# Kernel optimization log

Measured on AMD Instinct MI355X. Metric: run time of the kernel, lower is better.

Reference implementation:

```python
import jax, jax.numpy as jnp
import numpy as np

B, T, C = 8, 2048, 1024
EXP = 4
EPS = 1e-6


def rmsnorm(x, w):
    xf = x.astype(jnp.float32)
    y = xf * jax.lax.rsqrt(jnp.mean(xf * xf, axis=-1, keepdims=True) + EPS)
    return y.astype(x.dtype) * w


def setup_inputs() -> dict:
    key = jax.random.key(0)
    ks = jax.random.split(key, 8)
    x = jax.random.normal(ks[0], (B, T, C), dtype=jnp.float32)
    norm1_w = jnp.ones((C,), jnp.float32)
    norm2_w = jnp.ones((C,), jnp.float32)
    s1 = 1.0 / np.sqrt(C)
    s2 = 1.0 / np.sqrt(EXP * C)
    mlp1_w = jax.random.uniform(ks[1], (C, C), jnp.float32, -s1, s1)  # stored (in,out)
    mlp1_b = jax.random.uniform(ks[2], (C,), jnp.float32, -s1, s1)
    mlp2_w1 = jax.random.uniform(ks[3], (C, EXP * C), jnp.float32, -s1, s1)
    mlp2_b1 = jax.random.uniform(ks[4], (EXP * C,), jnp.float32, -s1, s1)
    mlp2_w2 = jax.random.uniform(ks[5], (EXP * C, C), jnp.float32, -s2, s2)
    mlp2_b2 = jax.random.uniform(ks[6], (C,), jnp.float32, -s2, s2)
    return {"x": x, "norm1_w": norm1_w, "mlp1_w": mlp1_w, "mlp1_b": mlp1_b,
            "norm2_w": norm2_w, "mlp2_w1": mlp2_w1, "mlp2_b1": mlp2_b1,
            "mlp2_w2": mlp2_w2, "mlp2_b2": mlp2_b2}


def reference(x, norm1_w, mlp1_w, mlp1_b, norm2_w, mlp2_w1, mlp2_b1, mlp2_w2, mlp2_b2):
    Tdim = x.shape[-2]
    # linear-RNN cumulative state with triangular-number scaler (faithful to source)
    state = jnp.cumsum(rmsnorm(x, norm1_w), axis=1)
    scaler = jnp.cumsum(jnp.arange(1, Tdim + 1, dtype=x.dtype))[None, :, None]
    state = state / scaler
    gate = jax.nn.sigmoid(jnp.einsum('btc,cd->btd', state, mlp1_w) + mlp1_b)
    out = gate * x
    h = rmsnorm(out, norm2_w)
    h = jax.nn.relu(jnp.einsum('btc,ce->bte', h, mlp2_w1) + mlp2_b1)
    out = jnp.einsum('bte,ec->btc', h, mlp2_w2) + mlp2_b2 + out
    return out
```

## Files before the change

### kernel.cpp

```cpp
#include <hip/hip_runtime.h>

__device__ __forceinline__ float bf2f(unsigned short u) {
    union { unsigned int i; float f; } v;
    v.i = ((unsigned int)u) << 16;
    return v.f;
}
__device__ __forceinline__ unsigned short f2bf(float f) {
    union { float f; unsigned int i; } v;
    v.f = f;
    unsigned int r = (v.i + 0x7fffu + ((v.i >> 16) & 1u)) >> 16;
    return (unsigned short)r;
}

typedef __attribute__((ext_vector_type(8))) short short8;
typedef __attribute__((ext_vector_type(4))) float floatx4;

#define GLOBAL_AS __attribute__((address_space(1)))
#define LDS_AS __attribute__((address_space(3)))

static constexpr int Bdim = 8;
static constexpr int Tdim = 2048;
static constexpr int Cdim = 1024;
static constexpr int Edim = 4096;
static constexpr int Mdim = Bdim * Tdim;

__global__ __launch_bounds__(256) void transpose_f2b(
    const float* __restrict__ src, unsigned short* __restrict__ dst, int K, int N) {
    __shared__ float tile[32][33];
    int n0 = blockIdx.x * 32;
    int k0 = blockIdx.y * 32;
    int tx = threadIdx.x & 31;
    int ty = threadIdx.x >> 5;
#pragma unroll
    for (int i = 0; i < 32; i += 8)
        tile[ty + i][tx] = src[(size_t)(k0 + ty + i) * N + n0 + tx];
    __syncthreads();
#pragma unroll
    for (int i = 0; i < 32; i += 8)
        dst[(size_t)(n0 + ty + i) * K + k0 + tx] = f2bf(tile[tx][ty + i]);
}

__global__ __launch_bounds__(256) void rms_inv_kernel(
    const float* __restrict__ x, float* __restrict__ rinv) {
    int row = blockIdx.x;
    int tid = threadIdx.x;
    float4 v = ((const float4*)(x + (size_t)row * Cdim))[tid];
    float s = v.x * v.x + v.y * v.y + v.z * v.z + v.w * v.w;
#pragma unroll
    for (int o = 32; o > 0; o >>= 1) s += __shfl_down(s, o, 64);
    __shared__ float ps[4];
    if ((tid & 63) == 0) ps[tid >> 6] = s;
    __syncthreads();
    if (tid == 0) {
        float tot = ps[0] + ps[1] + ps[2] + ps[3];
        rinv[row] = rsqrtf(tot * (1.0f / (float)Cdim) + 1e-6f);
    }
}

__global__ __launch_bounds__(256) void chunk_sums(
    const float* __restrict__ x, const float* __restrict__ rinv,
    const float* __restrict__ w, float* __restrict__ P) {
    int idx = blockIdx.x;
    int cb = idx & 3;
    int k = (idx >> 2) & 31;
    int b = idx >> 7;
    int c = cb * 256 + threadIdx.x;
    float wc = w[c];
    const float* base = x + ((size_t)b * Tdim + k * 64) * Cdim + c;
    const float* rbase = rinv + (size_t)b * Tdim + k * 64;
    float s = 0.f;
#pragma unroll 8
    for (int t = 0; t < 64; t++) s += base[(size_t)t * Cdim] * rbase[t];
    P[((size_t)b * 32 + k) * Cdim + c] = s * wc;
}

__global__ __launch_bounds__(256) void chunk_scan(float* __restrict__ P) {
    int g = blockIdx.x * 256 + threadIdx.x;
    int b = g >> 10;
    int c = g & 1023;
    float* p = P + (size_t)b * 32 * Cdim + c;
    float run = 0.f;
#pragma unroll
    for (int k = 0; k < 32; k++) {
        float v = p[(size_t)k * Cdim];
        p[(size_t)k * Cdim] = run;
        run += v;
    }
}

__global__ __launch_bounds__(256) void cumsum_state(
    const float* __restrict__ x, const float* __restrict__ rinv,
    const float* __restrict__ w, const float* __restrict__ P,
    unsigned short* __restrict__ state) {
    int idx = blockIdx.x;
    int cb = idx & 3;
    int k = (idx >> 2) & 31;
    int b = idx >> 7;
    int c = cb * 256 + threadIdx.x;
    float wc = w[c];
    float acc = P[((size_t)b * 32 + k) * Cdim + c];
    const float* base = x + ((size_t)b * Tdim + k * 64) * Cdim + c;
    const float* rbase = rinv + (size_t)b * Tdim + k * 64;
    unsigned short* sbase = state + ((size_t)b * Tdim + k * 64) * Cdim + c;
#pragma unroll 4
    for (int t = 0; t < 64; t++) {
        acc += base[(size_t)t * Cdim] * rbase[t] * wc;
        int tt = k * 64 + t;
        float inv = 2.0f / ((float)(tt + 1) * (float)(tt + 2));
        sbase[(size_t)t * Cdim] = f2bf(acc * inv);
    }
}

__global__ __launch_bounds__(256) void rmsnorm_f2b(
    const float* __restrict__ x, const float* __restrict__ w,
    unsigned short* __restrict__ y) {
    int row = blockIdx.x;
    int tid = threadIdx.x;
    float4 v = ((const float4*)(x + (size_t)row * Cdim))[tid];
    float s = v.x * v.x + v.y * v.y + v.z * v.z + v.w * v.w;
#pragma unroll
    for (int o = 32; o > 0; o >>= 1) s += __shfl_down(s, o, 64);
    __shared__ float ps[4];
    if ((tid & 63) == 0) ps[tid >> 6] = s;
    __syncthreads();
    float tot = ps[0] + ps[1] + ps[2] + ps[3];
    float r = rsqrtf(tot * (1.0f / (float)Cdim) + 1e-6f);
    float4 w4 = ((const float4*)w)[tid];
    ushort4 o;
    o.x = f2bf(v.x * r * w4.x);
    o.y = f2bf(v.y * r * w4.y);
    o.z = f2bf(v.z * r * w4.z);
    o.w = f2bf(v.w * r * w4.w);
    ((ushort4*)(y + (size_t)row * Cdim))[tid] = o;
}

template <int EPI>
__global__ __launch_bounds__(256) void gemm_bt(
    const unsigned short* __restrict__ A, const unsigned short* __restrict__ BT,
    const float* __restrict__ bias, const float* __restrict__ extra,
    void* __restrict__ Coutv, int M, int N, int K) {
    __shared__ __attribute__((aligned(16))) unsigned short As[2][128 * 32];
    __shared__ __attribute__((aligned(16))) unsigned short Bs[2][128 * 32];

    int tid = threadIdx.x;
    int bn = blockIdx.x, bm = blockIdx.y;
    int wave = tid >> 6, lane = tid & 63;
    int wm = (wave & 1) * 64, wn = (wave >> 1) * 64;
    int lrow = lane & 15;
    int lk = (lane >> 4) << 3;

    const unsigned short* Abase = A + (size_t)bm * 128 * K;
    const unsigned short* Bbase = BT + (size_t)bn * 128 * K;

    floatx4 acc[4][4] = {};

    int qrow = tid >> 2;
    int qcol = (tid & 3) << 3;
    const unsigned short* ArowLo = Abase + (size_t)qrow * K + qcol;
    const unsigned short* ArowHi = Abase + (size_t)(qrow + 64) * K + qcol;
    const unsigned short* BrowLo = Bbase + (size_t)qrow * K + qcol;
    const unsigned short* BrowHi = Bbase + (size_t)(qrow + 64) * K + qcol;

#define STAGE(buf, koff)                                                                   \
    do {                                                                                   \
        __builtin_amdgcn_global_load_lds((const GLOBAL_AS void*)(ArowLo + (koff)),         \
                                         (LDS_AS void*)(As[buf] + (size_t)tid * 8), 16, 0, 0); \
        __builtin_amdgcn_global_load_lds((const GLOBAL_AS void*)(ArowHi + (koff)),         \
                                         (LDS_AS void*)(As[buf] + (size_t)(tid + 256) * 8), 16, 0, 0); \
        __builtin_amdgcn_global_load_lds((const GLOBAL_AS void*)(BrowLo + (koff)),         \
                                         (LDS_AS void*)(Bs[buf] + (size_t)tid * 8), 16, 0, 0); \
        __builtin_amdgcn_global_load_lds((const GLOBAL_AS void*)(BrowHi + (koff)),         \
                                         (LDS_AS void*)(Bs[buf] + (size_t)(tid + 256) * 8), 16, 0, 0); \
    } while (0)

    int iters = K >> 5;
    STAGE(0, 0);
    for (int k = 0; k < iters; k++) {
        int cur = k & 1;
        __syncthreads();
        if (k + 1 < iters) STAGE(cur ^ 1, (k + 1) << 5);

        short8 af[4], bfr[4];
#pragma unroll
        for (int i = 0; i < 4; i++)
            af[i] = *(const short8*)(As[cur] + (wm + i * 16 + lrow) * 32 + lk);
#pragma unroll
        for (int j = 0; j < 4; j++)
            bfr[j] = *(const short8*)(Bs[cur] + (wn + j * 16 + lrow) * 32 + lk);
#pragma unroll
        for (int i = 0; i < 4; i++)
#pragma unroll
            for (int j = 0; j < 4; j++)
                acc[i][j] = __builtin_amdgcn_mfma_f32_16x16x32_bf16(af[i], bfr[j], acc[i][j], 0, 0, 0);
    }
#undef STAGE

    int crow = (lane >> 4) * 4;
    int ccol = lane & 15;
#pragma unroll
    for (int i = 0; i < 4; i++) {
#pragma unroll
        for (int j = 0; j < 4; j++) {
            size_t gm = (size_t)bm * 128 + wm + i * 16 + crow;
            size_t gn = (size_t)bn * 128 + wn + j * 16 + ccol;
            float bsv = bias[gn];
#pragma unroll
            for (int r = 0; r < 4; r++) {
                float v = acc[i][j][r] + bsv;
                size_t off = (gm + r) * (size_t)N + gn;
                if (EPI == 0) {
                    float g = 1.f / (1.f + __expf(-v));
                    ((float*)Coutv)[off] = g * extra[off];
                } else if (EPI == 1) {
                    ((unsigned short*)Coutv)[off] = f2bf(v > 0.f ? v : 0.f);
                } else {
                    ((float*)Coutv)[off] = v + extra[off];
                }
            }
        }
    }
}

extern "C" void kernel_launch(void* const* d_in, const int* in_sizes, int n_in,
                              void* d_out, int out_size, void* d_ws, size_t ws_size,
                              hipStream_t stream) {
    const float* x   = (const float*)d_in[0];
    const float* n1w = (const float*)d_in[1];
    const float* w1  = (const float*)d_in[2];
    const float* b1  = (const float*)d_in[3];
    const float* n2w = (const float*)d_in[4];
    const float* w21 = (const float*)d_in[5];
    const float* b21 = (const float*)d_in[6];
    const float* w22 = (const float*)d_in[7];
    const float* b22 = (const float*)d_in[8];
    float* out = (float*)d_out;

    char* ws = (char*)d_ws;
    const size_t MB = 1024ull * 1024ull;
    unsigned short* state = (unsigned short*)(ws);
    unsigned short* w1T   = (unsigned short*)(ws + 32 * MB);
    unsigned short* w21T  = (unsigned short*)(ws + 34 * MB);
    unsigned short* w22T  = (unsigned short*)(ws + 42 * MB);
    float* P              = (float*)(ws + 50 * MB);
    float* rinv           = (float*)(ws + 51 * MB);
    unsigned short* h     = (unsigned short*)(ws + 52 * MB);
    float* out1 = out;

    int slice_rows = Mdim;
    while (52 * MB + (size_t)slice_rows * Edim * 2 > ws_size && slice_rows > 1024)
        slice_rows >>= 1;

    transpose_f2b<<<dim3(Cdim / 32, Cdim / 32), 256, 0, stream>>>(w1, w1T, Cdim, Cdim);
    transpose_f2b<<<dim3(Edim / 32, Cdim / 32), 256, 0, stream>>>(w21, w21T, Cdim, Edim);
    transpose_f2b<<<dim3(Cdim / 32, Edim / 32), 256, 0, stream>>>(w22, w22T, Edim, Cdim);

    rms_inv_kernel<<<Mdim, 256, 0, stream>>>(x, rinv);

    chunk_sums<<<1024, 256, 0, stream>>>(x, rinv, n1w, P);
    chunk_scan<<<32, 256, 0, stream>>>(P);
    cumsum_state<<<1024, 256, 0, stream>>>(x, rinv, n1w, P, state);

    gemm_bt<0><<<dim3(Cdim / 128, Mdim / 128), 256, 0, stream>>>(
        state, w1T, b1, x, out1, Mdim, Cdim, Cdim);

    rmsnorm_f2b<<<Mdim, 256, 0, stream>>>(out1, n2w, state);

    for (int m0 = 0; m0 < Mdim; m0 += slice_rows) {
        gemm_bt<1><<<dim3(Edim / 128, slice_rows / 128), 256, 0, stream>>>(
            state + (size_t)m0 * Cdim, w21T, b21, nullptr, h, slice_rows, Edim, Cdim);
        gemm_bt<2><<<dim3(Cdim / 128, slice_rows / 128), 256, 0, stream>>>(
            h, w22T, b22, out1 + (size_t)m0 * Cdim, out + (size_t)m0 * Cdim,
            slice_rows, Cdim, Edim);
    }
}
```

Baseline: 649.3 us.

## Rewrite GEMM with 256x128 tiles, triple-buffered LDS, swizzle and XCD remap

Replaces the 128x128 double-buffered bf16 GEMM with a 512-thread 256x128 tile kernel. It uses BK=64, a three-stage LDS ring filled by global_load_lds, and an XOR swizzle to avoid LDS bank conflicts. A 1D grid is remapped so consecutive blocks land on the same XCD for L2 reuse, and loads are interleaved with MFMA halves using barriers and setprio. The aim is higher MFMA utilization and better latency hiding, at the cost of much more LDS (144KB) per block and tricky waitcnt ordering.

```diff
diff --git a/kernel.cpp b/kernel.cpp
--- a/kernel.cpp
+++ b/kernel.cpp
@@ -135,74 +135,129 @@
 }
 
 template <int EPI>
-__global__ __launch_bounds__(256) void gemm_bt(
+__global__ __launch_bounds__(512, 2) void gemm8(
     const unsigned short* __restrict__ A, const unsigned short* __restrict__ BT,
     const float* __restrict__ bias, const float* __restrict__ extra,
-    void* __restrict__ Coutv, int M, int N, int K) {
-    __shared__ __attribute__((aligned(16))) unsigned short As[2][128 * 32];
-    __shared__ __attribute__((aligned(16))) unsigned short Bs[2][128 * 32];
+    void* __restrict__ Coutv, int N, int K) {
+    __shared__ __attribute__((aligned(16))) unsigned short As[3][256 * 64];
+    __shared__ __attribute__((aligned(16))) unsigned short Bs[3][128 * 64];
 
     int tid = threadIdx.x;
-    int bn = blockIdx.x, bm = blockIdx.y;
-    int wave = tid >> 6, lane = tid & 63;
-    int wm = (wave & 1) * 64, wn = (wave >> 1) * 64;
+    int nbn = N >> 7;
+    int id = blockIdx.x;
+    int nwg = gridDim.x;
+    if ((nwg & 7) == 0) id = (id & 7) * (nwg >> 3) + (id >> 3);
+    int bn = id % nbn;
+    int bm = id / nbn;
+
+    int lane = tid & 63;
+    int w = tid >> 6;
+    int wm = w & 3;
+    int wn = w >> 2;
     int lrow = lane & 15;
-    int lk = (lane >> 4) << 3;
-
-    const unsigned short* Abase = A + (size_t)bm * 128 * K;
+    int l4 = lane >> 4;
+    int swz = lrow & 7;
+
+    const unsigned short* Abase = A + (size_t)bm * 256 * K;
     const unsigned short* Bbase = BT + (size_t)bn * 128 * K;
 
+    int sr = tid >> 3;
+    int col8 = (tid & 7) ^ (sr & 7);
+
+#define STAGE_A(sb, u, k0)                                                               \
+    __builtin_amdgcn_global_load_lds(                                                    \
+        (const GLOBAL_AS void*)(Abase + (size_t)((u) * 64 + sr) * K + (k0) + col8 * 8),  \
+        (LDS_AS void*)(As[sb] + (u) * 4096 + tid * 8), 16, 0, 0)
+#define STAGE_B(sb, u, k0)                                                               \
+    __builtin_amdgcn_global_load_lds(                                                    \
+        (const GLOBAL_AS void*)(Bbase + (size_t)((u) * 64 + sr) * K + (k0) + col8 * 8),  \
+        (LDS_AS void*)(Bs[sb] + (u) * 4096 + tid * 8), 16, 0, 0)
+
     floatx4 acc[4][4] = {};
-
-    int qrow = tid >> 2;
-    int qcol = (tid & 3) << 3;
-    const unsigned short* ArowLo = Abase + (size_t)qrow * K + qcol;
-    const unsigned short* ArowHi = Abase + (size_t)(qrow + 64) * K + qcol;
-    const unsigned short* BrowLo = Bbase + (size_t)qrow * K + qcol;
-    const unsigned short* BrowHi = Bbase + (size_t)(qrow + 64) * K + qcol;
-
-#define STAGE(buf, koff)                                                                   \
-    do {                                                                                   \
-        __builtin_amdgcn_global_load_lds((const GLOBAL_AS void*)(ArowLo + (koff)),         \
-                                         (LDS_AS void*)(As[buf] + (size_t)tid * 8), 16, 0, 0); \
-        __builtin_amdgcn_global_load_lds((const GLOBAL_AS void*)(ArowHi + (koff)),         \
-                                         (LDS_AS void*)(As[buf] + (size_t)(tid + 256) * 8), 16, 0, 0); \
-        __builtin_amdgcn_global_load_lds((const GLOBAL_AS void*)(BrowLo + (koff)),         \
-                                         (LDS_AS void*)(Bs[buf] + (size_t)tid * 8), 16, 0, 0); \
-        __builtin_amdgcn_global_load_lds((const GLOBAL_AS void*)(BrowHi + (koff)),         \
-                                         (LDS_AS void*)(Bs[buf] + (size_t)(tid + 256) * 8), 16, 0, 0); \
-    } while (0)
-
-    int iters = K >> 5;
-    STAGE(0, 0);
-    for (int k = 0; k < iters; k++) {
-        int cur = k & 1;
-        __syncthreads();
-        if (k + 1 < iters) STAGE(cur ^ 1, (k + 1) << 5);
-
-        short8 af[4], bfr[4];
+    int nt = K >> 6;
+
+    STAGE_A(0, 0, 0); STAGE_A(0, 1, 0); STAGE_A(0, 2, 0); STAGE_A(0, 3, 0);
+    STAGE_B(0, 0, 0); STAGE_B(0, 1, 0);
+    STAGE_A(1, 0, 64); STAGE_A(1, 1, 64); STAGE_A(1, 2, 64); STAGE_A(1, 3, 64);
+    STAGE_B(1, 0, 64); STAGE_B(1, 1, 64);
+    asm volatile("s_waitcnt vmcnt(6)" ::: "memory");
+    __builtin_amdgcn_s_barrier();
+
+    int buf = 0;
+    for (int t = 0; t < nt; t++) {
+        const unsigned short* Ab = As[buf];
+        const unsigned short* Bb = Bs[buf];
+        int sb = buf + 2; if (sb >= 3) sb -= 3;
+        int k2 = (t + 2) << 6;
+        bool st = (t + 2) < nt;
+
+        short8 af[4][2], bfr[2][2];
 #pragma unroll
         for (int i = 0; i < 4; i++)
-            af[i] = *(const short8*)(As[cur] + (wm + i * 16 + lrow) * 32 + lk);
-#pragma unroll
-        for (int j = 0; j < 4; j++)
-            bfr[j] = *(const short8*)(Bs[cur] + (wn + j * 16 + lrow) * 32 + lk);
+#pragma unroll
+            for (int ks = 0; ks < 2; ks++)
+                af[i][ks] = *(const short8*)(Ab + (wm * 64 + i * 16 + lrow) * 64 +
+                                             (((ks * 4 + l4) ^ swz) << 3));
+#pragma unroll
+        for (int j = 0; j < 2; j++)
+#pragma unroll
+            for (int ks = 0; ks < 2; ks++)
+                bfr[j][ks] = *(const short8*)(Bb + (wn * 64 + j * 16 + lrow) * 64 +
+                                              (((ks * 4 + l4) ^ swz) << 3));
+        if (st) { STAGE_A(sb, 0, k2); STAGE_A(sb, 1, k2); STAGE_A(sb, 2, k2); }
+        asm volatile("s_waitcnt lgkmcnt(8)" ::: "memory");
+        __builtin_amdgcn_s_barrier();
+        asm volatile("s_waitcnt lgkmcnt(0)" ::: "memory");
+        __builtin_amdgcn_s_setprio(1);
 #pragma unroll
         for (int i = 0; i < 4; i++)
 #pragma unroll
-            for (int j = 0; j < 4; j++)
-                acc[i][j] = __builtin_amdgcn_mfma_f32_16x16x32_bf16(af[i], bfr[j], acc[i][j], 0, 0, 0);
-    }
-#undef STAGE
-
-    int crow = (lane >> 4) * 4;
+            for (int j = 0; j < 2; j++)
+#pragma unroll
+                for (int ks = 0; ks < 2; ks++)
+                    acc[i][j] = __builtin_amdgcn_mfma_f32_16x16x32_bf16(
+                        af[i][ks], bfr[j][ks], acc[i][j], 0, 0, 0);
+        __builtin_amdgcn_s_setprio(0);
+        __builtin_amdgcn_s_barrier();
+
+#pragma unroll
+        for (int j = 0; j < 2; j++)
+#pragma unroll
+            for (int ks = 0; ks < 2; ks++)
+                bfr[j][ks] = *(const short8*)(Bb + (wn * 64 + (j + 2) * 16 + lrow) * 64 +
+                                              (((ks * 4 + l4) ^ swz) << 3));
+        if (st) { STAGE_A(sb, 3, k2); STAGE_B(sb, 0, k2); STAGE_B(sb, 1, k2); }
+        __builtin_amdgcn_s_barrier();
+        asm volatile("s_waitcnt lgkmcnt(0)" ::: "memory");
+        __builtin_amdgcn_s_setprio(1);
+#pragma unroll
+        for (int i = 0; i < 4; i++)
+#pragma unroll
+            for (int j = 0; j < 2; j++)
+#pragma unroll
+                for (int ks = 0; ks < 2; ks++)
+                    acc[i][j + 2] = __builtin_amdgcn_mfma_f32_16x16x32_bf16(
+                        af[i][ks], bfr[j][ks], acc[i][j + 2], 0, 0, 0);
+        __builtin_amdgcn_s_setprio(0);
+        if (t + 1 < nt) {
+            if (st) asm volatile("s_waitcnt vmcnt(6)" ::: "memory");
+            else    asm volatile("s_waitcnt vmcnt(0)" ::: "memory");
+        }
+        __builtin_amdgcn_s_barrier();
+
+        buf++; if (buf == 3) buf = 0;
+    }
+#undef STAGE_A
+#undef STAGE_B
+
+    int crow = l4 << 2;
     int ccol = lane & 15;
 #pragma unroll
     for (int i = 0; i < 4; i++) {
 #pragma unroll
         for (int j = 0; j < 4; j++) {
-            size_t gm = (size_t)bm * 128 + wm + i * 16 + crow;
-            size_t gn = (size_t)bn * 128 + wn + j * 16 + ccol;
+            size_t gm = (size_t)bm * 256 + wm * 64 + i * 16 + crow;
+            size_t gn = (size_t)bn * 128 + wn * 64 + j * 16 + ccol;
             float bsv = bias[gn];
 #pragma unroll
             for (int r = 0; r < 4; r++) {
@@ -260,16 +315,16 @@
     chunk_scan<<<32, 256, 0, stream>>>(P);
     cumsum_state<<<1024, 256, 0, stream>>>(x, rinv, n1w, P, state);
 
-    gemm_bt<0><<<dim3(Cdim / 128, Mdim / 128), 256, 0, stream>>>(
-        state, w1T, b1, x, out1, Mdim, Cdim, Cdim);
+    gemm8<0><<<dim3((Mdim / 256) * (Cdim / 128)), 512, 0, stream>>>(
+        state, w1T, b1, x, out1, Cdim, Cdim);
 
     rmsnorm_f2b<<<Mdim, 256, 0, stream>>>(out1, n2w, state);
 
     for (int m0 = 0; m0 < Mdim; m0 += slice_rows) {
-        gemm_bt<1><<<dim3(Edim / 128, slice_rows / 128), 256, 0, stream>>>(
-            state + (size_t)m0 * Cdim, w21T, b21, nullptr, h, slice_rows, Edim, Cdim);
-        gemm_bt<2><<<dim3(Cdim / 128, slice_rows / 128), 256, 0, stream>>>(
+        gemm8<1><<<dim3((slice_rows / 256) * (Edim / 128)), 512, 0, stream>>>(
+            state + (size_t)m0 * Cdim, w21T, b21, nullptr, h, Edim, Cdim);
+        gemm8<2><<<dim3((slice_rows / 256) * (Cdim / 128)), 512, 0, stream>>>(
             h, w22T, b22, out1 + (size_t)m0 * Cdim, out + (size_t)m0 * Cdim,
-            slice_rows, Cdim, Edim);
-    }
-}
+            Cdim, Edim);
+    }
+}
```

Result: faster. 612.0 us (-5.7%).
